# Kernel tuning notes

Measured on AMD Instinct MI355X. Metric: run time of the kernel, lower is better.

## Reference

```python
import jax, jax.numpy as jnp
import numpy as np

N_NODES = 50000
N_EDGES = 800000
NUM_GRAPHS = 128

def _sage_conv(x, src, dst, Wl, b, Wr):
    # PyG SAGEConv: lin_l(mean_{j in N(i)} x_j) + lin_r(x_i); bias only on lin_l
    msgs = x[src]                                             # [E, d] gather
    agg = jax.ops.segment_sum(msgs, dst, num_segments=N_NODES)
    deg = jax.ops.segment_sum(jnp.ones((src.shape[0],), x.dtype), dst,
                              num_segments=N_NODES)
    mean = agg / jnp.maximum(deg, 1.0)[:, None]               # [N, d]
    return mean @ Wl.T + b + x @ Wr.T

def setup_inputs() -> dict:
    key = jax.random.key(0)
    ks = jax.random.split(key, 12)
    d_in, d_h, d_out = 96, 96, 64
    def w(k, o, i):
        return jax.random.normal(k, (o, i), jnp.float32) * (1.0 / np.sqrt(i))
    return {
        "x": jax.random.normal(ks[0], (N_NODES, d_in), jnp.float32),
        "edge_index": jax.random.randint(ks[1], (2, N_EDGES), 0, N_NODES, jnp.int32),
        "batch": jnp.sort(jax.random.randint(ks[2], (N_NODES,), 0, NUM_GRAPHS, jnp.int32)),
        "Wl0": w(ks[3], d_h, d_in), "b0": jnp.zeros((d_h,), jnp.float32), "Wr0": w(ks[4], d_h, d_in),
        "Wl1": w(ks[5], d_h, d_h),  "b1": jnp.zeros((d_h,), jnp.float32), "Wr1": w(ks[6], d_h, d_h),
        "Wl2": w(ks[7], d_out, d_h), "b2": jnp.zeros((d_out,), jnp.float32), "Wr2": w(ks[8], d_out, d_h),
    }

def reference(x, edge_index, batch, Wl0, b0, Wr0, Wl1, b1, Wr1, Wl2, b2, Wr2):
    src, dst = edge_index[0], edge_index[1]
    h = jax.nn.relu(_sage_conv(x, src, dst, Wl0, b0, Wr0))   # dropout: eval mode -> identity
    h = jax.nn.relu(_sage_conv(h, src, dst, Wl1, b1, Wr1))
    h = _sage_conv(h, src, dst, Wl2, b2, Wr2)                 # [N, out]
    # global_mean_pool over graphs
    pooled = jax.ops.segment_sum(h, batch, num_segments=NUM_GRAPHS)
    cnt = jax.ops.segment_sum(jnp.ones((h.shape[0],), h.dtype), batch,
                              num_segments=NUM_GRAPHS)
    return pooled / jnp.maximum(cnt, 1.0)[:, None]            # [num_graphs, out]
```

## Files before the change

### kernel.cpp

```cpp
#include <hip/hip_runtime.h>
#include <stdint.h>
#include <stddef.h>

#define NN 50000
#define NP 50048
#define NE 800000
#define NG 128

#define NBKT 256
#define NPB 196
#define BCAP 4096
#define TILE_E 1536
#define PARTB 521
#define AGB 3125
#define TFB 782

typedef __attribute__((ext_vector_type(8))) short bf16x8;
typedef __attribute__((ext_vector_type(4))) float f32x4;
typedef __attribute__((ext_vector_type(4))) unsigned int u32x4;
typedef unsigned short ushort_t;
typedef unsigned int uint_t;

static __device__ inline ushort_t f2b(float f) {
    union { float f; uint_t u; } v; v.f = f;
    uint_t r = v.u + 0x7FFFu + ((v.u >> 16) & 1u);
    return (ushort_t)(r >> 16);
}
static __device__ inline float blo(uint_t u) {
    union { uint_t u; float f; } v; v.u = u << 16; return v.f;
}
static __device__ inline float bhi(uint_t u) {
    union { uint_t u; float f; } v; v.u = u & 0xFFFF0000u; return v.f;
}

__launch_bounds__(256) static __global__
void part_zero_kernel(const int* __restrict__ src, const int* __restrict__ dst,
                      int* __restrict__ bucket_cnt, uint_t* __restrict__ part,
                      float* __restrict__ out, const int* __restrict__ batch,
                      float* __restrict__ inv_cnt) {
    __shared__ int hist[NBKT];
    int tid = threadIdx.x;
    if (blockIdx.x < PARTB) {
        hist[tid] = 0;
        __syncthreads();
        int base = blockIdx.x * TILE_E;
        int end = min(base + TILE_E, NE);
        for (int i = base + tid; i < end; i += 256)
            atomicAdd(&hist[dst[i] / NPB], 1);
        __syncthreads();
        int r = atomicAdd(&bucket_cnt[tid], hist[tid]);
        __syncthreads();
        hist[tid] = r;
        __syncthreads();
        for (int i = base + tid; i < end; i += 256) {
            int s = src[i], d = dst[i];
            int b = d / NPB;
            int dl = d - b * NPB;
            int p = atomicAdd(&hist[b], 1);
            part[b * BCAP + p] = ((uint_t)dl << 16) | (uint_t)s;
        }
    } else {
        int gid = (blockIdx.x - PARTB) * 256 + tid;
        if (gid < NG * 64) out[gid] = 0.f;
        if (gid < NG) {
            int g = gid;
            int lo = 0, hi = NN;
            while (lo < hi) { int m = (lo + hi) >> 1; if (batch[m] < g) lo = m + 1; else hi = m; }
            int start = lo;
            hi = NN;
            while (lo < hi) { int m = (lo + hi) >> 1; if (batch[m] < g + 1) lo = m + 1; else hi = m; }
            inv_cnt[g] = 1.f / (float)max(lo - start, 1);
        }
    }
}

static __device__ void csr_build_body(int b, char* smem, const uint_t* __restrict__ part,
                                      const int* __restrict__ bucket_cnt,
                                      uint_t* __restrict__ od, ushort_t* __restrict__ csr) {
    uint_t* stage = (uint_t*)smem;
    ushort_t* cstage = (ushort_t*)(smem + 16384);
    int* cnt_s = (int*)(smem + 24576);
    int* scan_l = (int*)(smem + 25600);
    int* cur_l = (int*)(smem + 26624);
    int tid = threadIdx.x;
    int bc = bucket_cnt[tid];
    cnt_s[tid] = bc;
    scan_l[tid] = bc;
    __syncthreads();
    for (int off = 1; off < NBKT; off <<= 1) {
        int t = (tid >= off) ? scan_l[tid - off] : 0;
        __syncthreads();
        scan_l[tid] += t;
        __syncthreads();
    }
    int base = scan_l[b] - cnt_s[b];
    int n = cnt_s[b];
    __syncthreads();
    cnt_s[tid] = 0;
    __syncthreads();
    for (int i = tid; i < n; i += 256) {
        uint_t e = part[(size_t)b * BCAP + i];
        stage[i] = e;
        atomicAdd(&cnt_s[e >> 16], 1);
    }
    __syncthreads();
    int v = cnt_s[tid];
    scan_l[tid] = v;
    __syncthreads();
    for (int off = 1; off < NBKT; off <<= 1) {
        int t = (tid >= off) ? scan_l[tid - off] : 0;
        __syncthreads();
        scan_l[tid] += t;
        __syncthreads();
    }
    int ex = scan_l[tid] - v;
    scan_l[tid] = ex;
    cur_l[tid] = 0;
    __syncthreads();
    int g = b * NPB + tid;
    if (tid < NPB && g < NN) od[g] = ((uint_t)(base + ex) << 8) | (uint_t)v;
    for (int i = tid; i < n; i += 256) {
        uint_t e = stage[i];
        int dl = e >> 16;
        int p = atomicAdd(&cur_l[dl], 1);
        cstage[scan_l[dl] + p] = (ushort_t)(e & 0xFFFFu);
    }
    __syncthreads();
    for (int i = tid; i < n; i += 256) csr[base + i] = cstage[i];
}

template <int DOUT, int NT, bool FP32_IN>
static __device__ void transform_body(int bid, char* smem,
                                      const void* __restrict__ hin, const float* __restrict__ Wl,
                                      const float* __restrict__ bias, const float* __restrict__ Wr,
                                      ushort_t* __restrict__ tlc, ushort_t* __restrict__ trc) {
    constexpr int DIN = 96;
    short* w_s = (short*)smem;
    int tid = threadIdx.x;
    for (int idx = tid; idx < NT * 3 * 64; idx += 256) {
        int ci = idx >> 6, ln = idx & 63;
        int t = ci / 3, s = ci - 3 * t;
        int o = t * 16 + (ln & 15);
        int c0 = s * 32 + (ln >> 4) * 8;
        const float* wrow = (o < DOUT) ? (Wl + (size_t)o * DIN)
                                       : (Wr + (size_t)(o - DOUT) * DIN);
        float4 v0 = *(const float4*)(wrow + c0);
        float4 v1 = *(const float4*)(wrow + c0 + 4);
        bf16x8 pk;
        pk[0] = (short)f2b(v0.x); pk[1] = (short)f2b(v0.y);
        pk[2] = (short)f2b(v0.z); pk[3] = (short)f2b(v0.w);
        pk[4] = (short)f2b(v1.x); pk[5] = (short)f2b(v1.y);
        pk[6] = (short)f2b(v1.z); pk[7] = (short)f2b(v1.w);
        *(bf16x8*)&w_s[idx * 8] = pk;
    }
    int lane = tid & 63;
    int m0 = bid * 64 + (tid >> 6) * 16;
    int row = m0 + (lane & 15);
    bf16x8 a0, a1, a2;
    if (FP32_IN) {
        const float* xr = (const float*)hin + (size_t)min(row, NN - 1) * DIN + (lane >> 4) * 8;
#pragma unroll
        for (int s = 0; s < 3; s++) {
            float4 v0 = *(const float4*)(xr + s * 32);
            float4 v1 = *(const float4*)(xr + s * 32 + 4);
            bf16x8 pk;
            pk[0] = (short)f2b(v0.x); pk[1] = (short)f2b(v0.y);
            pk[2] = (short)f2b(v0.z); pk[3] = (short)f2b(v0.w);
            pk[4] = (short)f2b(v1.x); pk[5] = (short)f2b(v1.y);
            pk[6] = (short)f2b(v1.z); pk[7] = (short)f2b(v1.w);
            if (s == 0) a0 = pk; else if (s == 1) a1 = pk; else a2 = pk;
        }
    } else {
        const bf16x8* arow = (const bf16x8*)((const ushort_t*)hin + (size_t)row * DIN) + (lane >> 4);
        a0 = arow[0];
        a1 = arow[4];
        a2 = arow[8];
    }
    __syncthreads();
    const bf16x8* wp = (const bf16x8*)w_s + lane;
    f32x4 acc[NT];
#pragma unroll
    for (int t = 0; t < NT; t++) {
        acc[t] = (f32x4){0.f, 0.f, 0.f, 0.f};
        acc[t] = __builtin_amdgcn_mfma_f32_16x16x32_bf16(a0, wp[(t * 3 + 0) * 64], acc[t], 0, 0, 0);
        acc[t] = __builtin_amdgcn_mfma_f32_16x16x32_bf16(a1, wp[(t * 3 + 1) * 64], acc[t], 0, 0, 0);
        acc[t] = __builtin_amdgcn_mfma_f32_16x16x32_bf16(a2, wp[(t * 3 + 2) * 64], acc[t], 0, 0, 0);
    }
    int quad = lane >> 4, col = lane & 15;
#pragma unroll
    for (int t = 0; t < NT; t++) {
        int o = t * 16 + col;
        bool is_r = (o >= DOUT);
        float bv = is_r ? bias[o - DOUT] : 0.f;
        ushort_t* outp = is_r ? trc : tlc;
        int oo = is_r ? (o - DOUT) : o;
        int cch = oo >> 5, f = oo & 31;
        ushort_t* ob = outp + ((size_t)cch * NN) * 32 + f;
#pragma unroll
        for (int r = 0; r < 4; r++) {
            int node = m0 + quad * 4 + r;
            if (node < NN) ob[(size_t)node * 32] = f2b(acc[t][r] + bv);
        }
    }
}

__launch_bounds__(256) static __global__
void csr_tf0_kernel(const uint_t* __restrict__ part, const int* __restrict__ bucket_cnt,
                    uint_t* __restrict__ od, ushort_t* __restrict__ csr,
                    const float* __restrict__ x, const float* __restrict__ Wl0,
                    const float* __restrict__ b0, const float* __restrict__ Wr0,
                    ushort_t* __restrict__ tlc, ushort_t* __restrict__ trc) {
    __shared__ __align__(16) char smem[36864];
    if (blockIdx.x < NBKT)
        csr_build_body(blockIdx.x, smem, part, bucket_cnt, od, csr);
    else
        transform_body<96, 12, true>(blockIdx.x - NBKT, smem, x, Wl0, b0, Wr0, tlc, trc);
}

template <int DOUT, int NT>
__launch_bounds__(256, 4) static __global__
void transform_kernel(const ushort_t* __restrict__ hb, const float* __restrict__ Wl,
                      const float* __restrict__ bias, const float* __restrict__ Wr,
                      ushort_t* __restrict__ tlc, ushort_t* __restrict__ trc) {
    __shared__ __align__(16) char smem[NT * 3 * 64 * 8 * 2];
    transform_body<DOUT, NT, false>(blockIdx.x, smem, hb, Wl, bias, Wr, tlc, trc);
}

static __device__ inline void gather_accum(const uint_t* __restrict__ tl,
                                           const ushort_t* __restrict__ csr,
                                           int off, int dg, int ng, int fl,
                                           float* __restrict__ acc) {
    int k = 0;
    for (; k + 16 <= dg; k += 16) {
        int s0 = csr[off + k + ng];
        int s1 = csr[off + k + 4 + ng];
        int s2 = csr[off + k + 8 + ng];
        int s3 = csr[off + k + 12 + ng];
        uint4 a0 = *(const uint4*)(tl + (size_t)s0 * 16 + 4 * fl);
        uint4 a1 = *(const uint4*)(tl + (size_t)s1 * 16 + 4 * fl);
        uint4 a2 = *(const uint4*)(tl + (size_t)s2 * 16 + 4 * fl);
        uint4 a3 = *(const uint4*)(tl + (size_t)s3 * 16 + 4 * fl);
        acc[0] += (blo(a0.x) + blo(a1.x)) + (blo(a2.x) + blo(a3.x));
        acc[1] += (bhi(a0.x) + bhi(a1.x)) + (bhi(a2.x) + bhi(a3.x));
        acc[2] += (blo(a0.y) + blo(a1.y)) + (blo(a2.y) + blo(a3.y));
        acc[3] += (bhi(a0.y) + bhi(a1.y)) + (bhi(a2.y) + bhi(a3.y));
        acc[4] += (blo(a0.z) + blo(a1.z)) + (blo(a2.z) + blo(a3.z));
        acc[5] += (bhi(a0.z) + bhi(a1.z)) + (bhi(a2.z) + bhi(a3.z));
        acc[6] += (blo(a0.w) + blo(a1.w)) + (blo(a2.w) + blo(a3.w));
        acc[7] += (bhi(a0.w) + bhi(a1.w)) + (bhi(a2.w) + bhi(a3.w));
    }
    if (k + 8 <= dg) {
        int s0 = csr[off + k + ng];
        int s1 = csr[off + k + 4 + ng];
        uint4 a0 = *(const uint4*)(tl + (size_t)s0 * 16 + 4 * fl);
        uint4 a1 = *(const uint4*)(tl + (size_t)s1 * 16 + 4 * fl);
        acc[0] += blo(a0.x) + blo(a1.x); acc[1] += bhi(a0.x) + bhi(a1.x);
        acc[2] += blo(a0.y) + blo(a1.y); acc[3] += bhi(a0.y) + bhi(a1.y);
        acc[4] += blo(a0.z) + blo(a1.z); acc[5] += bhi(a0.z) + bhi(a1.z);
        acc[6] += blo(a0.w) + blo(a1.w); acc[7] += bhi(a0.w) + bhi(a1.w);
        k += 8;
    }
    if (k + 4 <= dg) {
        int s0 = csr[off + k + ng];
        uint4 a0 = *(const uint4*)(tl + (size_t)s0 * 16 + 4 * fl);
        acc[0] += blo(a0.x); acc[1] += bhi(a0.x);
        acc[2] += blo(a0.y); acc[3] += bhi(a0.y);
        acc[4] += blo(a0.z); acc[5] += bhi(a0.z);
        acc[6] += blo(a0.w); acc[7] += bhi(a0.w);
        k += 4;
    }
    if (ng < dg - k) {
        int s0 = csr[off + k + ng];
        uint4 a0 = *(const uint4*)(tl + (size_t)s0 * 16 + 4 * fl);
        acc[0] += blo(a0.x); acc[1] += bhi(a0.x);
        acc[2] += blo(a0.y); acc[3] += bhi(a0.y);
        acc[4] += blo(a0.z); acc[5] += bhi(a0.z);
        acc[6] += blo(a0.w); acc[7] += bhi(a0.w);
    }
}

template <int D>
__launch_bounds__(256) static __global__
void agg3_kernel(const ushort_t* __restrict__ tlc, const ushort_t* __restrict__ trc,
                 const uint_t* __restrict__ od, const ushort_t* __restrict__ csr,
                 ushort_t* __restrict__ outb) {
    int bx = blockIdx.x;
    int c = bx / AGB;
    int b = bx - c * AGB;
    int tid = threadIdx.x;
    int node = b * 16 + (tid >> 4);
    int lane = tid & 15;
    int ng = lane >> 2, fl = lane & 3;
    const uint_t* tl = (const uint_t*)tlc + (size_t)c * NN * 16;
    uint_t pd = od[node];
    int off = (int)(pd >> 8), dg = (int)(pd & 255u);
    float acc[8];
#pragma unroll
    for (int q = 0; q < 8; q++) acc[q] = 0.f;
    gather_accum(tl, csr, off, dg, ng, fl, acc);
#pragma unroll
    for (int q = 0; q < 8; q++) {
        acc[q] += __shfl_xor(acc[q], 4, 64);
        acc[q] += __shfl_xor(acc[q], 8, 64);
    }
    float s = 1.f / (float)max(dg, 1);
    u32x4 t = __builtin_nontemporal_load(
        (const u32x4*)((const uint_t*)trc + (size_t)c * NN * 16 + (size_t)node * 16 + 4 * fl));
    float v0 = fmaxf(fmaf(acc[0], s, blo(t.x)), 0.f);
    float v1 = fmaxf(fmaf(acc[1], s, bhi(t.x)), 0.f);
    float v2 = fmaxf(fmaf(acc[2], s, blo(t.y)), 0.f);
    float v3 = fmaxf(fmaf(acc[3], s, bhi(t.y)), 0.f);
    float v4 = fmaxf(fmaf(acc[4], s, blo(t.z)), 0.f);
    float v5 = fmaxf(fmaf(acc[5], s, bhi(t.z)), 0.f);
    float v6 = fmaxf(fmaf(acc[6], s, blo(t.w)), 0.f);
    float v7 = fmaxf(fmaf(acc[7], s, bhi(t.w)), 0.f);
    if (ng == 0) {
        u32x4 o;
        o.x = (uint_t)f2b(v0) | ((uint_t)f2b(v1) << 16);
        o.y = (uint_t)f2b(v2) | ((uint_t)f2b(v3) << 16);
        o.z = (uint_t)f2b(v4) | ((uint_t)f2b(v5) << 16);
        o.w = (uint_t)f2b(v6) | ((uint_t)f2b(v7) << 16);
        __builtin_nontemporal_store(
            o, (u32x4*)((uint_t*)outb + (size_t)node * (D / 2) + c * 16 + 4 * fl));
    }
}

__launch_bounds__(256) static __global__
void agg_pool_kernel(const ushort_t* __restrict__ tlc, const ushort_t* __restrict__ trc,
                     const uint_t* __restrict__ od, const ushort_t* __restrict__ csr,
                     const int* __restrict__ batch,
                     const float* __restrict__ inv_cnt, float* __restrict__ out) {
    __shared__ float hsum[16][32];
    __shared__ int gids[16];
    int bx = blockIdx.x;
    int c = bx / AGB;
    int b = bx - c * AGB;
    int tid = threadIdx.x;
    int nl = tid >> 4;
    int node = b * 16 + nl;
    int lane = tid & 15;
    int ng = lane >> 2, fl = lane & 3;
    if (tid < 16) gids[tid] = batch[b * 16 + tid];
    const uint_t* tl = (const uint_t*)tlc + (size_t)c * NN * 16;
    uint_t pd = od[node];
    int off = (int)(pd >> 8), dg = (int)(pd & 255u);
    float acc[8];
#pragma unroll
    for (int q = 0; q < 8; q++) acc[q] = 0.f;
    gather_accum(tl, csr, off, dg, ng, fl, acc);
#pragma unroll
    for (int q = 0; q < 8; q++) {
        acc[q] += __shfl_xor(acc[q], 4, 64);
        acc[q] += __shfl_xor(acc[q], 8, 64);
    }
    float s = 1.f / (float)max(dg, 1);
    u32x4 t = __builtin_nontemporal_load(
        (const u32x4*)((const uint_t*)trc + (size_t)c * NN * 16 + (size_t)node * 16 + 4 * fl));
    if (ng == 0) {
        hsum[nl][8 * fl + 0] = fmaf(acc[0], s, blo(t.x));
        hsum[nl][8 * fl + 1] = fmaf(acc[1], s, bhi(t.x));
        hsum[nl][8 * fl + 2] = fmaf(acc[2], s, blo(t.y));
        hsum[nl][8 * fl + 3] = fmaf(acc[3], s, bhi(t.y));
        hsum[nl][8 * fl + 4] = fmaf(acc[4], s, blo(t.z));
        hsum[nl][8 * fl + 5] = fmaf(acc[5], s, bhi(t.z));
        hsum[nl][8 * fl + 6] = fmaf(acc[6], s, blo(t.w));
        hsum[nl][8 * fl + 7] = fmaf(acc[7], s, bhi(t.w));
    }
    __syncthreads();
    if (tid < 32) {
        int gcur = gids[0];
        float ps = 0.f;
        for (int j = 0; j < 16; j++) {
            int g = gids[j];
            if (g != gcur) {
                atomicAdd(&out[gcur * 64 + c * 32 + tid], ps * inv_cnt[gcur]);
                ps = 0.f; gcur = g;
            }
            ps += hsum[j][tid];
        }
        atomicAdd(&out[gcur * 64 + c * 32 + tid], ps * inv_cnt[gcur]);
    }
}

extern "C" void kernel_launch(void* const* d_in, const int* in_sizes, int n_in,
                              void* d_out, int out_size, void* d_ws, size_t ws_size,
                              hipStream_t stream) {
    (void)in_sizes; (void)n_in; (void)out_size; (void)ws_size;
    const float* x   = (const float*)d_in[0];
    const int*   ei  = (const int*)d_in[1];
    const int*   bat = (const int*)d_in[2];
    const float* Wl0 = (const float*)d_in[3];
    const float* b0  = (const float*)d_in[4];
    const float* Wr0 = (const float*)d_in[5];
    const float* Wl1 = (const float*)d_in[6];
    const float* b1  = (const float*)d_in[7];
    const float* Wr1 = (const float*)d_in[8];
    const float* Wl2 = (const float*)d_in[9];
    const float* b2  = (const float*)d_in[10];
    const float* Wr2 = (const float*)d_in[11];
    float* out = (float*)d_out;
    const int* src = ei;
    const int* dst = ei + NE;

    char* p = (char*)d_ws;
    auto carve = [&](size_t bytes) -> char* {
        char* r = p;
        p += (bytes + 255) & ~(size_t)255;
        return r;
    };
    uint_t*   od     = (uint_t*)carve((size_t)NN * 4);
    int*      bucket_cnt = (int*)carve(NBKT * 4);
    float*    inv_cnt = (float*)carve(NG * 4);
    uint_t*   part   = (uint_t*)carve((size_t)NBKT * BCAP * 4);
    ushort_t* csr    = (ushort_t*)carve((size_t)NE * 2);
    ushort_t* h1b    = (ushort_t*)carve((size_t)NP * 96 * 2);
    ushort_t* h2b    = (ushort_t*)carve((size_t)NP * 96 * 2);
    ushort_t* tlc    = (ushort_t*)carve((size_t)3 * NN * 32 * 2);
    ushort_t* trc    = (ushort_t*)carve((size_t)3 * NN * 32 * 2);

    dim3 b256(256);
    hipMemsetAsync(bucket_cnt, 0, NBKT * 4, stream);

    part_zero_kernel<<<dim3(PARTB + 32), b256, 0, stream>>>(src, dst, bucket_cnt, part,
                                                            out, bat, inv_cnt);
    csr_tf0_kernel<<<dim3(NBKT + TFB), b256, 0, stream>>>(part, bucket_cnt, od, csr,
                                                          x, Wl0, b0, Wr0, tlc, trc);
    agg3_kernel<96><<<dim3(3 * AGB), b256, 0, stream>>>(tlc, trc, od, csr, h1b);
    transform_kernel<96, 12><<<dim3(TFB), b256, 0, stream>>>(h1b, Wl1, b1, Wr1, tlc, trc);
    agg3_kernel<96><<<dim3(3 * AGB), b256, 0, stream>>>(tlc, trc, od, csr, h2b);
    transform_kernel<64, 8><<<dim3(TFB), b256, 0, stream>>>(h2b, Wl2, b2, Wr2, tlc, trc);
    agg_pool_kernel<<<dim3(2 * AGB), b256, 0, stream>>>(tlc, trc, od, csr, bat,
                                                        inv_cnt, out);
}
```

Before: 237.3 us.

## Process two nodes per 16-lane group with zero-row padded branchless gather

Each 16-thread group now aggregates two destination nodes at once, issuing eight independent row loads per iteration to raise memory-level parallelism, and halves the number of aggregation blocks. The tail handling is replaced by a branchless loop that redirects out-of-range neighbor slots to a dedicated zero row appended to each feature chunk (row stride becomes NNR). The cost is wasted loads on the zero row when the two nodes' degrees differ or are not multiples of 16, plus extra register pressure from doubled accumulators.

```diff
diff --git a/kernel.cpp b/kernel.cpp
--- a/kernel.cpp
+++ b/kernel.cpp
@@ -3,6 +3,7 @@
 #include <stddef.h>
 
 #define NN 50000
+#define NNR 50008
 #define NP 50048
 #define NE 800000
 #define NG 128
@@ -12,8 +13,9 @@
 #define BCAP 4096
 #define TILE_E 1536
 #define PARTB 521
-#define AGB 3125
+#define AGB2 1563
 #define TFB 782
+#define ZR NN
 
 typedef __attribute__((ext_vector_type(8))) short bf16x8;
 typedef __attribute__((ext_vector_type(4))) float f32x4;
@@ -21,6 +23,8 @@
 typedef unsigned short ushort_t;
 typedef unsigned int uint_t;
 
+#define CS_U ((size_t)NNR * 16)
+
 static __device__ inline ushort_t f2b(float f) {
     union { float f; uint_t u; } v; v.f = f;
     uint_t r = v.u + 0x7FFFu + ((v.u >> 16) & 1u);
@@ -37,7 +41,7 @@
 void part_zero_kernel(const int* __restrict__ src, const int* __restrict__ dst,
                       int* __restrict__ bucket_cnt, uint_t* __restrict__ part,
                       float* __restrict__ out, const int* __restrict__ batch,
-                      float* __restrict__ inv_cnt) {
+                      float* __restrict__ inv_cnt, uint_t* __restrict__ tlz) {
     __shared__ int hist[NBKT];
     int tid = threadIdx.x;
     if (blockIdx.x < PARTB) {
@@ -62,6 +66,10 @@
     } else {
         int gid = (blockIdx.x - PARTB) * 256 + tid;
         if (gid < NG * 64) out[gid] = 0.f;
+        if (gid < 48) {
+            int cc = gid >> 4, ii = gid & 15;
+            tlz[(size_t)cc * CS_U + (size_t)ZR * 16 + ii] = 0u;
+        }
         if (gid < NG) {
             int g = gid;
             int lo = 0, hi = NN;
@@ -195,7 +203,7 @@
         ushort_t* outp = is_r ? trc : tlc;
         int oo = is_r ? (o - DOUT) : o;
         int cch = oo >> 5, f = oo & 31;
-        ushort_t* ob = outp + ((size_t)cch * NN) * 32 + f;
+        ushort_t* ob = outp + ((size_t)cch * NNR) * 32 + f;
 #pragma unroll
         for (int r = 0; r < 4; r++) {
             int node = m0 + quad * 4 + r;
@@ -226,56 +234,42 @@
     transform_body<DOUT, NT, false>(blockIdx.x, smem, hb, Wl, bias, Wr, tlc, trc);
 }
 
-static __device__ inline void gather_accum(const uint_t* __restrict__ tl,
-                                           const ushort_t* __restrict__ csr,
-                                           int off, int dg, int ng, int fl,
-                                           float* __restrict__ acc) {
-    int k = 0;
-    for (; k + 16 <= dg; k += 16) {
-        int s0 = csr[off + k + ng];
-        int s1 = csr[off + k + 4 + ng];
-        int s2 = csr[off + k + 8 + ng];
-        int s3 = csr[off + k + 12 + ng];
-        uint4 a0 = *(const uint4*)(tl + (size_t)s0 * 16 + 4 * fl);
-        uint4 a1 = *(const uint4*)(tl + (size_t)s1 * 16 + 4 * fl);
-        uint4 a2 = *(const uint4*)(tl + (size_t)s2 * 16 + 4 * fl);
-        uint4 a3 = *(const uint4*)(tl + (size_t)s3 * 16 + 4 * fl);
-        acc[0] += (blo(a0.x) + blo(a1.x)) + (blo(a2.x) + blo(a3.x));
-        acc[1] += (bhi(a0.x) + bhi(a1.x)) + (bhi(a2.x) + bhi(a3.x));
-        acc[2] += (blo(a0.y) + blo(a1.y)) + (blo(a2.y) + blo(a3.y));
-        acc[3] += (bhi(a0.y) + bhi(a1.y)) + (bhi(a2.y) + bhi(a3.y));
-        acc[4] += (blo(a0.z) + blo(a1.z)) + (blo(a2.z) + blo(a3.z));
-        acc[5] += (bhi(a0.z) + bhi(a1.z)) + (bhi(a2.z) + bhi(a3.z));
-        acc[6] += (blo(a0.w) + blo(a1.w)) + (blo(a2.w) + blo(a3.w));
-        acc[7] += (bhi(a0.w) + bhi(a1.w)) + (bhi(a2.w) + bhi(a3.w));
-    }
-    if (k + 8 <= dg) {
-        int s0 = csr[off + k + ng];
-        int s1 = csr[off + k + 4 + ng];
-        uint4 a0 = *(const uint4*)(tl + (size_t)s0 * 16 + 4 * fl);
-        uint4 a1 = *(const uint4*)(tl + (size_t)s1 * 16 + 4 * fl);
-        acc[0] += blo(a0.x) + blo(a1.x); acc[1] += bhi(a0.x) + bhi(a1.x);
-        acc[2] += blo(a0.y) + blo(a1.y); acc[3] += bhi(a0.y) + bhi(a1.y);
-        acc[4] += blo(a0.z) + blo(a1.z); acc[5] += bhi(a0.z) + bhi(a1.z);
-        acc[6] += blo(a0.w) + blo(a1.w); acc[7] += bhi(a0.w) + bhi(a1.w);
-        k += 8;
-    }
-    if (k + 4 <= dg) {
-        int s0 = csr[off + k + ng];
-        uint4 a0 = *(const uint4*)(tl + (size_t)s0 * 16 + 4 * fl);
-        acc[0] += blo(a0.x); acc[1] += bhi(a0.x);
-        acc[2] += blo(a0.y); acc[3] += bhi(a0.y);
-        acc[4] += blo(a0.z); acc[5] += bhi(a0.z);
-        acc[6] += blo(a0.w); acc[7] += bhi(a0.w);
-        k += 4;
-    }
-    if (ng < dg - k) {
-        int s0 = csr[off + k + ng];
-        uint4 a0 = *(const uint4*)(tl + (size_t)s0 * 16 + 4 * fl);
-        acc[0] += blo(a0.x); acc[1] += bhi(a0.x);
-        acc[2] += blo(a0.y); acc[3] += bhi(a0.y);
-        acc[4] += blo(a0.z); acc[5] += bhi(a0.z);
-        acc[6] += blo(a0.w); acc[7] += bhi(a0.w);
+#define ACC4(acc, r0, r1, r2, r3)                                   \
+    acc[0] += (blo(r0.x) + blo(r1.x)) + (blo(r2.x) + blo(r3.x));    \
+    acc[1] += (bhi(r0.x) + bhi(r1.x)) + (bhi(r2.x) + bhi(r3.x));    \
+    acc[2] += (blo(r0.y) + blo(r1.y)) + (blo(r2.y) + blo(r3.y));    \
+    acc[3] += (bhi(r0.y) + bhi(r1.y)) + (bhi(r2.y) + bhi(r3.y));    \
+    acc[4] += (blo(r0.z) + blo(r1.z)) + (blo(r2.z) + blo(r3.z));    \
+    acc[5] += (bhi(r0.z) + bhi(r1.z)) + (bhi(r2.z) + bhi(r3.z));    \
+    acc[6] += (blo(r0.w) + blo(r1.w)) + (blo(r2.w) + blo(r3.w));    \
+    acc[7] += (bhi(r0.w) + bhi(r1.w)) + (bhi(r2.w) + bhi(r3.w));
+
+static __device__ inline void gather2(const uint_t* __restrict__ tl,
+                                      const ushort_t* __restrict__ csr,
+                                      int offA, int dgA, int offB, int dgB,
+                                      int ng, int fl,
+                                      float* __restrict__ accA, float* __restrict__ accB) {
+    int kmax = max(dgA, dgB);
+    for (int k = 0; k < kmax; k += 16) {
+        int sl0 = k + ng, sl1 = k + 4 + ng, sl2 = k + 8 + ng, sl3 = k + 12 + ng;
+        int ia0 = csr[offA + sl0], ia1 = csr[offA + sl1];
+        int ia2 = csr[offA + sl2], ia3 = csr[offA + sl3];
+        int ib0 = csr[offB + sl0], ib1 = csr[offB + sl1];
+        int ib2 = csr[offB + sl2], ib3 = csr[offB + sl3];
+        ia0 = sl0 < dgA ? ia0 : ZR;  ia1 = sl1 < dgA ? ia1 : ZR;
+        ia2 = sl2 < dgA ? ia2 : ZR;  ia3 = sl3 < dgA ? ia3 : ZR;
+        ib0 = sl0 < dgB ? ib0 : ZR;  ib1 = sl1 < dgB ? ib1 : ZR;
+        ib2 = sl2 < dgB ? ib2 : ZR;  ib3 = sl3 < dgB ? ib3 : ZR;
+        uint4 rA0 = *(const uint4*)(tl + (size_t)ia0 * 16 + 4 * fl);
+        uint4 rA1 = *(const uint4*)(tl + (size_t)ia1 * 16 + 4 * fl);
+        uint4 rA2 = *(const uint4*)(tl + (size_t)ia2 * 16 + 4 * fl);
+        uint4 rA3 = *(const uint4*)(tl + (size_t)ia3 * 16 + 4 * fl);
+        uint4 rB0 = *(const uint4*)(tl + (size_t)ib0 * 16 + 4 * fl);
+        uint4 rB1 = *(const uint4*)(tl + (size_t)ib1 * 16 + 4 * fl);
+        uint4 rB2 = *(const uint4*)(tl + (size_t)ib2 * 16 + 4 * fl);
+        uint4 rB3 = *(const uint4*)(tl + (size_t)ib3 * 16 + 4 * fl);
+        ACC4(accA, rA0, rA1, rA2, rA3)
+        ACC4(accB, rB0, rB1, rB2, rB3)
     }
 }
 
@@ -285,43 +279,56 @@
                  const uint_t* __restrict__ od, const ushort_t* __restrict__ csr,
                  ushort_t* __restrict__ outb) {
     int bx = blockIdx.x;
-    int c = bx / AGB;
-    int b = bx - c * AGB;
+    int c = bx / AGB2;
+    int b = bx - c * AGB2;
     int tid = threadIdx.x;
-    int node = b * 16 + (tid >> 4);
+    int g16 = tid >> 4;
+    int nodeA = b * 32 + g16 * 2;
+    int nodeB = nodeA + 1;
     int lane = tid & 15;
     int ng = lane >> 2, fl = lane & 3;
-    const uint_t* tl = (const uint_t*)tlc + (size_t)c * NN * 16;
-    uint_t pd = od[node];
-    int off = (int)(pd >> 8), dg = (int)(pd & 255u);
-    float acc[8];
-#pragma unroll
-    for (int q = 0; q < 8; q++) acc[q] = 0.f;
-    gather_accum(tl, csr, off, dg, ng, fl, acc);
+    const uint_t* tl = (const uint_t*)tlc + (size_t)c * CS_U;
+    uint_t pdA = od[min(nodeA, NN - 1)];
+    uint_t pdB = od[min(nodeB, NN - 1)];
+    int offA = (int)(pdA >> 8), dgA = (nodeA < NN) ? (int)(pdA & 255u) : 0;
+    int offB = (int)(pdB >> 8), dgB = (nodeB < NN) ? (int)(pdB & 255u) : 0;
+    float accA[8], accB[8];
+#pragma unroll
+    for (int q = 0; q < 8; q++) { accA[q] = 0.f; accB[q] = 0.f; }
+    gather2(tl, csr, offA, dgA, offB, dgB, ng, fl, accA, accB);
 #pragma unroll
     for (int q = 0; q < 8; q++) {
-        acc[q] += __shfl_xor(acc[q], 4, 64);
-        acc[q] += __shfl_xor(acc[q], 8, 64);
-    }
-    float s = 1.f / (float)max(dg, 1);
-    u32x4 t = __builtin_nontemporal_load(
-        (const u32x4*)((const uint_t*)trc + (size_t)c * NN * 16 + (size_t)node * 16 + 4 * fl));
-    float v0 = fmaxf(fmaf(acc[0], s, blo(t.x)), 0.f);
-    float v1 = fmaxf(fmaf(acc[1], s, bhi(t.x)), 0.f);
-    float v2 = fmaxf(fmaf(acc[2], s, blo(t.y)), 0.f);
-    float v3 = fmaxf(fmaf(acc[3], s, bhi(t.y)), 0.f);
-    float v4 = fmaxf(fmaf(acc[4], s, blo(t.z)), 0.f);
-    float v5 = fmaxf(fmaf(acc[5], s, bhi(t.z)), 0.f);
-    float v6 = fmaxf(fmaf(acc[6], s, blo(t.w)), 0.f);
-    float v7 = fmaxf(fmaf(acc[7], s, bhi(t.w)), 0.f);
-    if (ng == 0) {
-        u32x4 o;
-        o.x = (uint_t)f2b(v0) | ((uint_t)f2b(v1) << 16);
-        o.y = (uint_t)f2b(v2) | ((uint_t)f2b(v3) << 16);
-        o.z = (uint_t)f2b(v4) | ((uint_t)f2b(v5) << 16);
-        o.w = (uint_t)f2b(v6) | ((uint_t)f2b(v7) << 16);
-        __builtin_nontemporal_store(
-            o, (u32x4*)((uint_t*)outb + (size_t)node * (D / 2) + c * 16 + 4 * fl));
+        accA[q] += __shfl_xor(accA[q], 4, 64);
+        accA[q] += __shfl_xor(accA[q], 8, 64);
+        accB[q] += __shfl_xor(accB[q], 4, 64);
+        accB[q] += __shfl_xor(accB[q], 8, 64);
+    }
+    const uint_t* trb = (const uint_t*)trc + (size_t)c * CS_U;
+#pragma unroll
+    for (int half = 0; half < 2; half++) {
+        int node = half ? nodeB : nodeA;
+        float* acc = half ? accB : accA;
+        int dg = half ? dgB : dgA;
+        float s = 1.f / (float)max(dg, 1);
+        u32x4 t = __builtin_nontemporal_load(
+            (const u32x4*)(trb + (size_t)min(node, NN - 1) * 16 + 4 * fl));
+        float v0 = fmaxf(fmaf(acc[0], s, blo(t.x)), 0.f);
+        float v1 = fmaxf(fmaf(acc[1], s, bhi(t.x)), 0.f);
+        float v2 = fmaxf(fmaf(acc[2], s, blo(t.y)), 0.f);
+        float v3 = fmaxf(fmaf(acc[3], s, bhi(t.y)), 0.f);
+        float v4 = fmaxf(fmaf(acc[4], s, blo(t.z)), 0.f);
+        float v5 = fmaxf(fmaf(acc[5], s, bhi(t.z)), 0.f);
+        float v6 = fmaxf(fmaf(acc[6], s, blo(t.w)), 0.f);
+        float v7 = fmaxf(fmaf(acc[7], s, bhi(t.w)), 0.f);
+        if (ng == 0 && node < NN) {
+            u32x4 o;
+            o.x = (uint_t)f2b(v0) | ((uint_t)f2b(v1) << 16);
+            o.y = (uint_t)f2b(v2) | ((uint_t)f2b(v3) << 16);
+            o.z = (uint_t)f2b(v4) | ((uint_t)f2b(v5) << 16);
+            o.w = (uint_t)f2b(v6) | ((uint_t)f2b(v7) << 16);
+            __builtin_nontemporal_store(
+                o, (u32x4*)((uint_t*)outb + (size_t)node * (D / 2) + c * 16 + 4 * fl));
+        }
     }
 }
 
@@ -330,47 +337,61 @@
                      const uint_t* __restrict__ od, const ushort_t* __restrict__ csr,
                      const int* __restrict__ batch,
                      const float* __restrict__ inv_cnt, float* __restrict__ out) {
-    __shared__ float hsum[16][32];
-    __shared__ int gids[16];
+    __shared__ float hsum[32][32];
+    __shared__ int gids[32];
     int bx = blockIdx.x;
-    int c = bx / AGB;
-    int b = bx - c * AGB;
+    int c = bx / AGB2;
+    int b = bx - c * AGB2;
     int tid = threadIdx.x;
-    int nl = tid >> 4;
-    int node = b * 16 + nl;
+    int g16 = tid >> 4;
+    int nodeA = b * 32 + g16 * 2;
+    int nodeB = nodeA + 1;
     int lane = tid & 15;
     int ng = lane >> 2, fl = lane & 3;
-    if (tid < 16) gids[tid] = batch[b * 16 + tid];
-    const uint_t* tl = (const uint_t*)tlc + (size_t)c * NN * 16;
-    uint_t pd = od[node];
-    int off = (int)(pd >> 8), dg = (int)(pd & 255u);
-    float acc[8];
-#pragma unroll
-    for (int q = 0; q < 8; q++) acc[q] = 0.f;
-    gather_accum(tl, csr, off, dg, ng, fl, acc);
+    if (tid < 32) gids[tid] = batch[min(b * 32 + tid, NN - 1)];
+    const uint_t* tl = (const uint_t*)tlc + (size_t)c * CS_U;
+    uint_t pdA = od[min(nodeA, NN - 1)];
+    uint_t pdB = od[min(nodeB, NN - 1)];
+    int offA = (int)(pdA >> 8), dgA = (nodeA < NN) ? (int)(pdA & 255u) : 0;
+    int offB = (int)(pdB >> 8), dgB = (nodeB < NN) ? (int)(pdB & 255u) : 0;
+    float accA[8], accB[8];
+#pragma unroll
+    for (int q = 0; q < 8; q++) { accA[q] = 0.f; accB[q] = 0.f; }
+    gather2(tl, csr, offA, dgA, offB, dgB, ng, fl, accA, accB);
 #pragma unroll
     for (int q = 0; q < 8; q++) {
-        acc[q] += __shfl_xor(acc[q], 4, 64);
-        acc[q] += __shfl_xor(acc[q], 8, 64);
-    }
-    float s = 1.f / (float)max(dg, 1);
-    u32x4 t = __builtin_nontemporal_load(
-        (const u32x4*)((const uint_t*)trc + (size_t)c * NN * 16 + (size_t)node * 16 + 4 * fl));
-    if (ng == 0) {
-        hsum[nl][8 * fl + 0] = fmaf(acc[0], s, blo(t.x));
-        hsum[nl][8 * fl + 1] = fmaf(acc[1], s, bhi(t.x));
-        hsum[nl][8 * fl + 2] = fmaf(acc[2], s, blo(t.y));
-        hsum[nl][8 * fl + 3] = fmaf(acc[3], s, bhi(t.y));
-        hsum[nl][8 * fl + 4] = fmaf(acc[4], s, blo(t.z));
-        hsum[nl][8 * fl + 5] = fmaf(acc[5], s, bhi(t.z));
-        hsum[nl][8 * fl + 6] = fmaf(acc[6], s, blo(t.w));
-        hsum[nl][8 * fl + 7] = fmaf(acc[7], s, bhi(t.w));
+        accA[q] += __shfl_xor(accA[q], 4, 64);
+        accA[q] += __shfl_xor(accA[q], 8, 64);
+        accB[q] += __shfl_xor(accB[q], 4, 64);
+        accB[q] += __shfl_xor(accB[q], 8, 64);
+    }
+    const uint_t* trb = (const uint_t*)trc + (size_t)c * CS_U;
+#pragma unroll
+    for (int half = 0; half < 2; half++) {
+        int node = half ? nodeB : nodeA;
+        float* acc = half ? accB : accA;
+        int dg = half ? dgB : dgA;
+        int nl = g16 * 2 + half;
+        float s = 1.f / (float)max(dg, 1);
+        u32x4 t = __builtin_nontemporal_load(
+            (const u32x4*)(trb + (size_t)min(node, NN - 1) * 16 + 4 * fl));
+        if (ng == 0) {
+            bool v = node < NN;
+            hsum[nl][8 * fl + 0] = v ? fmaf(acc[0], s, blo(t.x)) : 0.f;
+            hsum[nl][8 * fl + 1] = v ? fmaf(acc[1], s, bhi(t.x)) : 0.f;
+            hsum[nl][8 * fl + 2] = v ? fmaf(acc[2], s, blo(t.y)) : 0.f;
+            hsum[nl][8 * fl + 3] = v ? fmaf(acc[3], s, bhi(t.y)) : 0.f;
+            hsum[nl][8 * fl + 4] = v ? fmaf(acc[4], s, blo(t.z)) : 0.f;
+            hsum[nl][8 * fl + 5] = v ? fmaf(acc[5], s, bhi(t.z)) : 0.f;
+            hsum[nl][8 * fl + 6] = v ? fmaf(acc[6], s, blo(t.w)) : 0.f;
+            hsum[nl][8 * fl + 7] = v ? fmaf(acc[7], s, bhi(t.w)) : 0.f;
+        }
     }
     __syncthreads();
     if (tid < 32) {
         int gcur = gids[0];
         float ps = 0.f;
-        for (int j = 0; j < 16; j++) {
+        for (int j = 0; j < 32; j++) {
             int g = gids[j];
             if (g != gcur) {
                 atomicAdd(&out[gcur * 64 + c * 32 + tid], ps * inv_cnt[gcur]);
@@ -415,20 +436,20 @@
     ushort_t* csr    = (ushort_t*)carve((size_t)NE * 2);
     ushort_t* h1b    = (ushort_t*)carve((size_t)NP * 96 * 2);
     ushort_t* h2b    = (ushort_t*)carve((size_t)NP * 96 * 2);
-    ushort_t* tlc    = (ushort_t*)carve((size_t)3 * NN * 32 * 2);
-    ushort_t* trc    = (ushort_t*)carve((size_t)3 * NN * 32 * 2);
+    ushort_t* tlc    = (ushort_t*)carve((size_t)3 * NNR * 32 * 2);
+    ushort_t* trc    = (ushort_t*)carve((size_t)3 * NNR * 32 * 2);
 
     dim3 b256(256);
     hipMemsetAsync(bucket_cnt, 0, NBKT * 4, stream);
 
     part_zero_kernel<<<dim3(PARTB + 32), b256, 0, stream>>>(src, dst, bucket_cnt, part,
-                                                            out, bat, inv_cnt);
+                                                            out, bat, inv_cnt, (uint_t*)tlc);
     csr_tf0_kernel<<<dim3(NBKT + TFB), b256, 0, stream>>>(part, bucket_cnt, od, csr,
                                                           x, Wl0, b0, Wr0, tlc, trc);
-    agg3_kernel<96><<<dim3(3 * AGB), b256, 0, stream>>>(tlc, trc, od, csr, h1b);
+    agg3_kernel<96><<<dim3(3 * AGB2), b256, 0, stream>>>(tlc, trc, od, csr, h1b);
     transform_kernel<96, 12><<<dim3(TFB), b256, 0, stream>>>(h1b, Wl1, b1, Wr1, tlc, trc);
-    agg3_kernel<96><<<dim3(3 * AGB), b256, 0, stream>>>(tlc, trc, od, csr, h2b);
+    agg3_kernel<96><<<dim3(3 * AGB2), b256, 0, stream>>>(tlc, trc, od, csr, h2b);
     transform_kernel<64, 8><<<dim3(TFB), b256, 0, stream>>>(h2b, Wl2, b2, Wr2, tlc, trc);
-    agg_pool_kernel<<<dim3(2 * AGB), b256, 0, stream>>>(tlc, trc, od, csr, bat,
-                                                        inv_cnt, out);
-}
+    agg_pool_kernel<<<dim3(2 * AGB2), b256, 0, stream>>>(tlc, trc, od, csr, bat,
+                                                         inv_cnt, out);
+}
```

Result: no change. 241.3 us (+1.7%).

## Fuse neighbor aggregation with next-layer MFMA transform via shared-memory staging

Applied to the files above, without the earlier changes.

Merges each aggregation kernel with the following transform kernel. Every 64-node block gathers all three 32-feature chunks into shared memory as bf16, then runs the MFMA transform straight from LDS. Ping-pong tl/tr buffers are used so the next layer's outputs do not overwrite inputs still being read. This drops the intermediate h buffer round trip and two launches. In exchange, the gather parallelism falls from 9375 blocks of 16 nodes to 782 blocks each looping over 12 node groups, which may hurt latency hiding for the random gathers.

```diff
diff --git a/kernel.cpp b/kernel.cpp
--- a/kernel.cpp
+++ b/kernel.cpp
@@ -129,11 +129,11 @@
     for (int i = tid; i < n; i += 256) csr[base + i] = cstage[i];
 }
 
-template <int DOUT, int NT, bool FP32_IN>
-static __device__ void transform_body(int bid, char* smem,
-                                      const void* __restrict__ hin, const float* __restrict__ Wl,
-                                      const float* __restrict__ bias, const float* __restrict__ Wr,
-                                      ushort_t* __restrict__ tlc, ushort_t* __restrict__ trc) {
+template <int DOUT, int NT>
+static __device__ void mfma_store(int bid, char* smem, bf16x8 a0, bf16x8 a1, bf16x8 a2,
+                                  const float* __restrict__ Wl, const float* __restrict__ bias,
+                                  const float* __restrict__ Wr,
+                                  ushort_t* __restrict__ tlc, ushort_t* __restrict__ trc) {
     constexpr int DIN = 96;
     short* w_s = (short*)smem;
     int tid = threadIdx.x;
@@ -153,12 +153,52 @@
         pk[6] = (short)f2b(v1.z); pk[7] = (short)f2b(v1.w);
         *(bf16x8*)&w_s[idx * 8] = pk;
     }
+    __syncthreads();
     int lane = tid & 63;
     int m0 = bid * 64 + (tid >> 6) * 16;
-    int row = m0 + (lane & 15);
-    bf16x8 a0, a1, a2;
-    if (FP32_IN) {
-        const float* xr = (const float*)hin + (size_t)min(row, NN - 1) * DIN + (lane >> 4) * 8;
+    const bf16x8* wp = (const bf16x8*)w_s + lane;
+    f32x4 acc[NT];
+#pragma unroll
+    for (int t = 0; t < NT; t++) {
+        acc[t] = (f32x4){0.f, 0.f, 0.f, 0.f};
+        acc[t] = __builtin_amdgcn_mfma_f32_16x16x32_bf16(a0, wp[(t * 3 + 0) * 64], acc[t], 0, 0, 0);
+        acc[t] = __builtin_amdgcn_mfma_f32_16x16x32_bf16(a1, wp[(t * 3 + 1) * 64], acc[t], 0, 0, 0);
+        acc[t] = __builtin_amdgcn_mfma_f32_16x16x32_bf16(a2, wp[(t * 3 + 2) * 64], acc[t], 0, 0, 0);
+    }
+    int quad = lane >> 4, col = lane & 15;
+#pragma unroll
+    for (int t = 0; t < NT; t++) {
+        int o = t * 16 + col;
+        bool is_r = (o >= DOUT);
+        float bv = is_r ? bias[o - DOUT] : 0.f;
+        ushort_t* outp = is_r ? trc : tlc;
+        int oo = is_r ? (o - DOUT) : o;
+        int cch = oo >> 5, f = oo & 31;
+        ushort_t* ob = outp + ((size_t)cch * NN) * 32 + f;
+#pragma unroll
+        for (int r = 0; r < 4; r++) {
+            int node = m0 + quad * 4 + r;
+            if (node < NN) ob[(size_t)node * 32] = f2b(acc[t][r] + bv);
+        }
+    }
+}
+
+__launch_bounds__(256) static __global__
+void csr_tf0_kernel(const uint_t* __restrict__ part, const int* __restrict__ bucket_cnt,
+                    uint_t* __restrict__ od, ushort_t* __restrict__ csr,
+                    const float* __restrict__ x, const float* __restrict__ Wl0,
+                    const float* __restrict__ b0, const float* __restrict__ Wr0,
+                    ushort_t* __restrict__ tlc, ushort_t* __restrict__ trc) {
+    __shared__ __align__(16) char smem[36864];
+    if (blockIdx.x < NBKT) {
+        csr_build_body(blockIdx.x, smem, part, bucket_cnt, od, csr);
+    } else {
+        int bid = blockIdx.x - NBKT;
+        int tid = threadIdx.x;
+        int lane = tid & 63;
+        int row = bid * 64 + (tid >> 6) * 16 + (lane & 15);
+        const float* xr = x + (size_t)min(row, NN - 1) * 96 + (lane >> 4) * 8;
+        bf16x8 a0, a1, a2;
 #pragma unroll
         for (int s = 0; s < 3; s++) {
             float4 v0 = *(const float4*)(xr + s * 32);
@@ -170,60 +210,8 @@
             pk[6] = (short)f2b(v1.z); pk[7] = (short)f2b(v1.w);
             if (s == 0) a0 = pk; else if (s == 1) a1 = pk; else a2 = pk;
         }
-    } else {
-        const bf16x8* arow = (const bf16x8*)((const ushort_t*)hin + (size_t)row * DIN) + (lane >> 4);
-        a0 = arow[0];
-        a1 = arow[4];
-        a2 = arow[8];
-    }
-    __syncthreads();
-    const bf16x8* wp = (const bf16x8*)w_s + lane;
-    f32x4 acc[NT];
-#pragma unroll
-    for (int t = 0; t < NT; t++) {
-        acc[t] = (f32x4){0.f, 0.f, 0.f, 0.f};
-        acc[t] = __builtin_amdgcn_mfma_f32_16x16x32_bf16(a0, wp[(t * 3 + 0) * 64], acc[t], 0, 0, 0);
-        acc[t] = __builtin_amdgcn_mfma_f32_16x16x32_bf16(a1, wp[(t * 3 + 1) * 64], acc[t], 0, 0, 0);
-        acc[t] = __builtin_amdgcn_mfma_f32_16x16x32_bf16(a2, wp[(t * 3 + 2) * 64], acc[t], 0, 0, 0);
-    }
-    int quad = lane >> 4, col = lane & 15;
-#pragma unroll
-    for (int t = 0; t < NT; t++) {
-        int o = t * 16 + col;
-        bool is_r = (o >= DOUT);
-        float bv = is_r ? bias[o - DOUT] : 0.f;
-        ushort_t* outp = is_r ? trc : tlc;
-        int oo = is_r ? (o - DOUT) : o;
-        int cch = oo >> 5, f = oo & 31;
-        ushort_t* ob = outp + ((size_t)cch * NN) * 32 + f;
-#pragma unroll
-        for (int r = 0; r < 4; r++) {
-            int node = m0 + quad * 4 + r;
-            if (node < NN) ob[(size_t)node * 32] = f2b(acc[t][r] + bv);
-        }
-    }
-}
-
-__launch_bounds__(256) static __global__
-void csr_tf0_kernel(const uint_t* __restrict__ part, const int* __restrict__ bucket_cnt,
-                    uint_t* __restrict__ od, ushort_t* __restrict__ csr,
-                    const float* __restrict__ x, const float* __restrict__ Wl0,
-                    const float* __restrict__ b0, const float* __restrict__ Wr0,
-                    ushort_t* __restrict__ tlc, ushort_t* __restrict__ trc) {
-    __shared__ __align__(16) char smem[36864];
-    if (blockIdx.x < NBKT)
-        csr_build_body(blockIdx.x, smem, part, bucket_cnt, od, csr);
-    else
-        transform_body<96, 12, true>(blockIdx.x - NBKT, smem, x, Wl0, b0, Wr0, tlc, trc);
-}
-
-template <int DOUT, int NT>
-__launch_bounds__(256, 4) static __global__
-void transform_kernel(const ushort_t* __restrict__ hb, const float* __restrict__ Wl,
-                      const float* __restrict__ bias, const float* __restrict__ Wr,
-                      ushort_t* __restrict__ tlc, ushort_t* __restrict__ trc) {
-    __shared__ __align__(16) char smem[NT * 3 * 64 * 8 * 2];
-    transform_body<DOUT, NT, false>(blockIdx.x, smem, hb, Wl, bias, Wr, tlc, trc);
+        mfma_store<96, 12>(bid, smem, a0, a1, a2, Wl0, b0, Wr0, tlc, trc);
+    }
 }
 
 static __device__ inline void gather_accum(const uint_t* __restrict__ tl,
@@ -279,50 +267,70 @@
     }
 }
 
-template <int D>
-__launch_bounds__(256) static __global__
-void agg3_kernel(const ushort_t* __restrict__ tlc, const ushort_t* __restrict__ trc,
-                 const uint_t* __restrict__ od, const ushort_t* __restrict__ csr,
-                 ushort_t* __restrict__ outb) {
-    int bx = blockIdx.x;
-    int c = bx / AGB;
-    int b = bx - c * AGB;
+template <int DOUT, int NT>
+__launch_bounds__(256, 4) static __global__
+void aggtf_kernel(const ushort_t* __restrict__ tlin, const ushort_t* __restrict__ trin,
+                  const uint_t* __restrict__ od, const ushort_t* __restrict__ csr,
+                  const float* __restrict__ Wl, const float* __restrict__ bias,
+                  const float* __restrict__ Wr,
+                  ushort_t* __restrict__ tlo, ushort_t* __restrict__ tro) {
+    constexpr int SMEM = (NT * 3 * 64 * 16 > 12288) ? NT * 3 * 64 * 16 : 12288;
+    __shared__ __align__(16) char smem[SMEM];
+    uint_t* hbuf = (uint_t*)smem;
     int tid = threadIdx.x;
-    int node = b * 16 + (tid >> 4);
-    int lane = tid & 15;
-    int ng = lane >> 2, fl = lane & 3;
-    const uint_t* tl = (const uint_t*)tlc + (size_t)c * NN * 16;
-    uint_t pd = od[node];
-    int off = (int)(pd >> 8), dg = (int)(pd & 255u);
-    float acc[8];
-#pragma unroll
-    for (int q = 0; q < 8; q++) acc[q] = 0.f;
-    gather_accum(tl, csr, off, dg, ng, fl, acc);
-#pragma unroll
-    for (int q = 0; q < 8; q++) {
-        acc[q] += __shfl_xor(acc[q], 4, 64);
-        acc[q] += __shfl_xor(acc[q], 8, 64);
-    }
-    float s = 1.f / (float)max(dg, 1);
-    u32x4 t = __builtin_nontemporal_load(
-        (const u32x4*)((const uint_t*)trc + (size_t)c * NN * 16 + (size_t)node * 16 + 4 * fl));
-    float v0 = fmaxf(fmaf(acc[0], s, blo(t.x)), 0.f);
-    float v1 = fmaxf(fmaf(acc[1], s, bhi(t.x)), 0.f);
-    float v2 = fmaxf(fmaf(acc[2], s, blo(t.y)), 0.f);
-    float v3 = fmaxf(fmaf(acc[3], s, bhi(t.y)), 0.f);
-    float v4 = fmaxf(fmaf(acc[4], s, blo(t.z)), 0.f);
-    float v5 = fmaxf(fmaf(acc[5], s, bhi(t.z)), 0.f);
-    float v6 = fmaxf(fmaf(acc[6], s, blo(t.w)), 0.f);
-    float v7 = fmaxf(fmaf(acc[7], s, bhi(t.w)), 0.f);
-    if (ng == 0) {
-        u32x4 o;
-        o.x = (uint_t)f2b(v0) | ((uint_t)f2b(v1) << 16);
-        o.y = (uint_t)f2b(v2) | ((uint_t)f2b(v3) << 16);
-        o.z = (uint_t)f2b(v4) | ((uint_t)f2b(v5) << 16);
-        o.w = (uint_t)f2b(v6) | ((uint_t)f2b(v7) << 16);
-        __builtin_nontemporal_store(
-            o, (u32x4*)((uint_t*)outb + (size_t)node * (D / 2) + c * 16 + 4 * fl));
-    }
+    int bid = blockIdx.x;
+    int lane16 = tid & 15;
+    int ng = lane16 >> 2, fl = lane16 & 3;
+    for (int c = 0; c < 3; c++) {
+        const uint_t* tl = (const uint_t*)tlin + (size_t)c * NN * 16;
+        const uint_t* trb = (const uint_t*)trin + (size_t)c * NN * 16;
+#pragma unroll
+        for (int g = 0; g < 4; g++) {
+            int nloc = g * 16 + (tid >> 4);
+            int node = bid * 64 + nloc;
+            uint_t pd = od[min(node, NN - 1)];
+            int off = (int)(pd >> 8);
+            int dg = (node < NN) ? (int)(pd & 255u) : 0;
+            float acc[8];
+#pragma unroll
+            for (int q = 0; q < 8; q++) acc[q] = 0.f;
+            gather_accum(tl, csr, off, dg, ng, fl, acc);
+#pragma unroll
+            for (int q = 0; q < 8; q++) {
+                acc[q] += __shfl_xor(acc[q], 4, 64);
+                acc[q] += __shfl_xor(acc[q], 8, 64);
+            }
+            float s = 1.f / (float)max(dg, 1);
+            u32x4 t = __builtin_nontemporal_load(
+                (const u32x4*)(trb + (size_t)min(node, NN - 1) * 16 + 4 * fl));
+            if (ng == 0) {
+                float v0 = fmaxf(fmaf(acc[0], s, blo(t.x)), 0.f);
+                float v1 = fmaxf(fmaf(acc[1], s, bhi(t.x)), 0.f);
+                float v2 = fmaxf(fmaf(acc[2], s, blo(t.y)), 0.f);
+                float v3 = fmaxf(fmaf(acc[3], s, bhi(t.y)), 0.f);
+                float v4 = fmaxf(fmaf(acc[4], s, blo(t.z)), 0.f);
+                float v5 = fmaxf(fmaf(acc[5], s, bhi(t.z)), 0.f);
+                float v6 = fmaxf(fmaf(acc[6], s, blo(t.w)), 0.f);
+                float v7 = fmaxf(fmaf(acc[7], s, bhi(t.w)), 0.f);
+                u32x4 o;
+                o.x = (uint_t)f2b(v0) | ((uint_t)f2b(v1) << 16);
+                o.y = (uint_t)f2b(v2) | ((uint_t)f2b(v3) << 16);
+                o.z = (uint_t)f2b(v4) | ((uint_t)f2b(v5) << 16);
+                o.w = (uint_t)f2b(v6) | ((uint_t)f2b(v7) << 16);
+                *(u32x4*)&hbuf[nloc * 48 + c * 16 + 4 * fl] = o;
+            }
+        }
+    }
+    __syncthreads();
+    int lane = tid & 63;
+    int row = (tid >> 6) * 16 + (lane & 15);
+    const ushort_t* hb = (const ushort_t*)smem;
+    const ushort_t* hr = hb + row * 96 + (lane >> 4) * 8;
+    bf16x8 a0 = *(const bf16x8*)(hr);
+    bf16x8 a1 = *(const bf16x8*)(hr + 32);
+    bf16x8 a2 = *(const bf16x8*)(hr + 64);
+    __syncthreads();
+    mfma_store<DOUT, NT>(bid, smem, a0, a1, a2, Wl, bias, Wr, tlo, tro);
 }
 
 __launch_bounds__(256) static __global__
@@ -413,10 +421,10 @@
     float*    inv_cnt = (float*)carve(NG * 4);
     uint_t*   part   = (uint_t*)carve((size_t)NBKT * BCAP * 4);
     ushort_t* csr    = (ushort_t*)carve((size_t)NE * 2);
-    ushort_t* h1b    = (ushort_t*)carve((size_t)NP * 96 * 2);
-    ushort_t* h2b    = (ushort_t*)carve((size_t)NP * 96 * 2);
-    ushort_t* tlc    = (ushort_t*)carve((size_t)3 * NN * 32 * 2);
-    ushort_t* trc    = (ushort_t*)carve((size_t)3 * NN * 32 * 2);
+    ushort_t* tlcA   = (ushort_t*)carve((size_t)3 * NN * 32 * 2);
+    ushort_t* trcA   = (ushort_t*)carve((size_t)3 * NN * 32 * 2);
+    ushort_t* tlcB   = (ushort_t*)carve((size_t)3 * NN * 32 * 2);
+    ushort_t* trcB   = (ushort_t*)carve((size_t)3 * NN * 32 * 2);
 
     dim3 b256(256);
     hipMemsetAsync(bucket_cnt, 0, NBKT * 4, stream);
@@ -424,11 +432,11 @@
     part_zero_kernel<<<dim3(PARTB + 32), b256, 0, stream>>>(src, dst, bucket_cnt, part,
                                                             out, bat, inv_cnt);
     csr_tf0_kernel<<<dim3(NBKT + TFB), b256, 0, stream>>>(part, bucket_cnt, od, csr,
-                                                          x, Wl0, b0, Wr0, tlc, trc);
-    agg3_kernel<96><<<dim3(3 * AGB), b256, 0, stream>>>(tlc, trc, od, csr, h1b);
-    transform_kernel<96, 12><<<dim3(TFB), b256, 0, stream>>>(h1b, Wl1, b1, Wr1, tlc, trc);
-    agg3_kernel<96><<<dim3(3 * AGB), b256, 0, stream>>>(tlc, trc, od, csr, h2b);
-    transform_kernel<64, 8><<<dim3(TFB), b256, 0, stream>>>(h2b, Wl2, b2, Wr2, tlc, trc);
-    agg_pool_kernel<<<dim3(2 * AGB), b256, 0, stream>>>(tlc, trc, od, csr, bat,
+                                                          x, Wl0, b0, Wr0, tlcA, trcA);
+    aggtf_kernel<96, 12><<<dim3(TFB), b256, 0, stream>>>(tlcA, trcA, od, csr,
+                                                         Wl1, b1, Wr1, tlcB, trcB);
+    aggtf_kernel<64, 8><<<dim3(TFB), b256, 0, stream>>>(tlcB, trcB, od, csr,
+                                                        Wl2, b2, Wr2, tlcA, trcA);
+    agg_pool_kernel<<<dim3(2 * AGB), b256, 0, stream>>>(tlcA, trcA, od, csr, bat,
                                                         inv_cnt, out);
 }
```

After: 288.9 us. 1.22x slower.
